# Performance work log

Measured on AMD Instinct MI355X. Metric: run time of the kernel, lower is better.

Reference implementation:

```python
import jax, jax.numpy as jnp
import numpy as np

K = 8              # kernel_size
C_IN = 3           # input_channels
HID = 256          # hidden_state_size
MID = 256          # mid_layer_size
N_MAIN = 4         # num_main_layers
N_CLS = 1000       # num_classes
N_PIX = K * K      # num_pixel_values
IN_VEC = 2 + 1 + N_PIX * C_IN + HID   # 451
OUT_VEC = 2 + 1 + HID                 # 259
B, H, W = 128, 256, 256


def _lin_init(k, fan_in, fan_out):
    kw, kb = jax.random.split(k)
    bound = 1.0 / np.sqrt(fan_in)
    w = jax.random.uniform(kw, (fan_in, fan_out), jnp.float32, -bound, bound)
    b = jax.random.uniform(kb, (fan_out,), jnp.float32, -bound, bound)
    return w, b


def setup_inputs() -> dict:
    key = jax.random.key(0)
    ks = jax.random.split(key, 16)
    image = jax.random.normal(ks[0], (B, C_IN, H, W), jnp.float32)
    locations = jax.random.uniform(ks[1], (B, 2), jnp.float32)
    scales = jax.random.uniform(ks[2], (B, 1), jnp.float32)
    hidden_state = jax.random.normal(ks[3], (B, HID), jnp.float32)
    w0, b0 = _lin_init(ks[4], IN_VEC, MID)
    rws, rbs = [], []
    for i in range(N_MAIN):
        w, b = _lin_init(jax.random.fold_in(ks[5], i), MID, MID)
        rws.append(w); rbs.append(b)
    rw = jnp.stack(rws); rb = jnp.stack(rbs)          # [4,MID,MID], [4,MID]
    wf, bf = _lin_init(ks[6], MID, OUT_VEC)
    cw0, cb0 = _lin_init(ks[7], HID, MID)
    crw, crb = _lin_init(ks[8], MID, MID)
    cw1, cb1 = _lin_init(ks[9], MID, N_CLS)
    return {"image": image, "locations": locations, "scales": scales,
            "hidden_state": hidden_state, "w0": w0, "b0": b0, "rw": rw,
            "rb": rb, "wf": wf, "bf": bf, "cw0": cw0, "cb0": cb0,
            "crw": crw, "crb": crb, "cw1": cw1, "cb1": cb1}


def fourier_interp_2d(image, sample_points):
    """Band-limited (NUDFT) interpolation of image at continuous points.
    image: [B,C,H,W]; sample_points: [B,N,2] in normalized [0,1) (ij order).
    Returns [B,N,C]."""
    Bsz, C, Hh, Ww = image.shape
    F = jnp.fft.fft2(image)                       # [B,C,H,W] complex
    fy = jnp.fft.fftfreq(Hh) * Hh                 # integer freqs [H]
    fx = jnp.fft.fftfreq(Ww) * Ww                 # integer freqs [W]
    y = sample_points[..., 0]                     # [B,N]
    x = sample_points[..., 1]
    two_pi_i = 2j * jnp.pi
    Ey = jnp.exp(two_pi_i * y[..., None] * fy)    # [B,N,H]
    Ex = jnp.exp(two_pi_i * x[..., None] * fx)    # [B,N,W]
    tmp = jnp.einsum('bchw,bnh->bcnw', F, Ey)     # dominant compute
    vals = jnp.einsum('bcnw,bnw->bcn', tmp, Ex).real / (Hh * Ww)
    return jnp.transpose(vals, (0, 2, 1))         # [B,N,C]


def reference(image, locations, scales, hidden_state,
              w0, b0, rw, rb, wf, bf, cw0, cb0, crw, crb, cw1, cb1):
    Bsz = image.shape[0]
    # base meshgrid: [K,K,2], ij indexing, values arange(K)/K
    g = jnp.arange(K, dtype=image.dtype) / K
    mesh = jnp.stack(jnp.meshgrid(g, g, indexing='ij'), axis=-1)  # [K,K,2]
    coords = mesh[None] - locations[:, None, None, :]             # [B,K,K,2]
    coords = coords * scales[:, None, None, :]
    coords = coords.reshape(Bsz, N_PIX, 2)
    pix = fourier_interp_2d(image, coords)                        # [B,N,C]
    pix = pix.reshape(Bsz, N_PIX * C_IN)
    inp = jnp.concatenate([locations, scales, pix, hidden_state], axis=-1)
    h = inp @ w0 + b0
    for i in range(N_MAIN):
        h = jax.nn.relu(h @ rw[i] + rb[i] + h)
    out = jnp.tanh(h @ wf + bf)                                   # [B,OUT_VEC]
    new_loc = locations + out[:, :2]
    new_scale = scales + out[:, 2:3]
    new_hidden = hidden_state + out[:, 3:]
    c = jax.nn.relu(new_hidden @ cw0 + cb0)
    c = jax.nn.relu(c @ crw + crb + c)
    preds = jax.nn.softmax(c @ cw1 + cb1, axis=-1)
    # concat all outputs: [B, 2+1+HID+N_CLS]
    return jnp.concatenate([new_loc, new_scale, new_hidden, preds], axis=-1)
```

## Files before the change

kernel.cpp:

```cpp
#include <hip/hip_runtime.h>
#include <math.h>

#define BB 128
#define OUTROW 1259

typedef float vf4 __attribute__((ext_vector_type(4)));

__device__ __forceinline__ ushort f2b(float x) {
    unsigned u = __float_as_uint(x);
    unsigned r = (u + 0x7FFFu + ((u >> 16) & 1u)) >> 16;
    return (ushort)r;
}
__device__ __forceinline__ uint pack2(float lo, float hi) {
    return (uint)f2b(lo) | ((uint)f2b(hi) << 16);
}
__device__ __forceinline__ float dot2bf(uint a, uint b, float c) {
    float d;
    asm("v_dot2_f32_bf16 %0, %1, %2, %3" : "=v"(d) : "v"(a), "v"(b), "v"(c));
    return d;
}

#define OFF_W0   0u
#define OFF_RW   122880u
#define OFF_CW0  385024u
#define OFF_CRW  450560u
#define OFF_WF   516096u
#define OFF_CW1  582656u
#define N_TOT    838656u

__device__ __forceinline__ void dirichlet_ab(float t, float& A, float& Bv) {
    float r = t - rintf(t);
    float s256 = sinpif(256.0f * r);
    Bv = s256 * (1.0f / 256.0f);
    if (fabsf(r) < 1e-6f) {
        A = 1.0f;
    } else {
        float sp = sinpif(r), cp = cospif(r);
        A = Bv * cp / sp;
    }
}

__global__ __launch_bounds__(256) void interp_convert_kernel(
    const float* __restrict__ image, const float* __restrict__ loc,
    const float* __restrict__ scl, float* __restrict__ pix,
    const float* __restrict__ w0, const float* __restrict__ rw,
    const float* __restrict__ wf, const float* __restrict__ cw0,
    const float* __restrict__ crw, const float* __restrict__ cw1,
    ushort* __restrict__ bfa)
{
    __shared__ float U[256 * 16];
    __shared__ float V[16 * 260];
    __shared__ float T[16 * 260];

    int bid = blockIdx.x;
    int tid = threadIdx.x;

    if (bid >= 384) {
        unsigned g = (unsigned)(bid - 384) * 256u + (unsigned)tid;
        for (unsigned i = g; i < N_TOT; i += 512u * 256u) {
            unsigned j = i;
            if (j < 122880u) {
                unsigned kp = j >> 9, r = j & 511u, c = r >> 1, k = 2u*kp + (r & 1u);
                bfa[OFF_W0 + j] = (k < 451u) ? f2b(w0[k * 256u + c]) : (ushort)0;
            } else if (j < 385024u) {
                unsigned jj = j - 122880u;
                unsigned kp = jj >> 9, r = jj & 511u, c = r >> 1, k = 2u*kp + (r & 1u);
                bfa[OFF_RW + jj] = f2b(rw[k * 256u + c]);
            } else if (j < 450560u) {
                unsigned jj = j - 385024u;
                unsigned kp = jj >> 9, r = jj & 511u, c = r >> 1, k = 2u*kp + (r & 1u);
                bfa[OFF_CW0 + jj] = f2b(cw0[k * 256u + c]);
            } else if (j < 516096u) {
                unsigned jj = j - 450560u;
                unsigned kp = jj >> 9, r = jj & 511u, c = r >> 1, k = 2u*kp + (r & 1u);
                bfa[OFF_CRW + jj] = f2b(crw[k * 256u + c]);
            } else if (j < 582656u) {
                unsigned jj = j - 516096u;
                unsigned kp = jj / 520u, r = jj - kp * 520u, c = r >> 1, k = 2u*kp + (r & 1u);
                bfa[OFF_WF + jj] = (c < 259u) ? f2b(wf[k * 259u + c]) : (ushort)0;
            } else {
                unsigned jj = j - 582656u;
                unsigned kp = jj / 2000u, r = jj - kp * 2000u, c = r >> 1, k = 2u*kp + (r & 1u);
                bfa[OFF_CW1 + jj] = f2b(cw1[k * 1000u + c]);
            }
        }
        return;
    }

    int b = bid / 3, c = bid % 3;
    float l0 = loc[2 * b], l1 = loc[2 * b + 1], sc = scl[b];

    {
        int p = tid;
        float tp = (float)p * (1.0f / 256.0f);
        #pragma unroll
        for (int iy = 0; iy < 8; ++iy) {
            float A, Bv;
            float y = ((float)iy * 0.125f - l0) * sc;
            dirichlet_ab(y - tp, A, Bv);
            int w = iy >> 1, o = iy & 1;
            U[p * 16 + w * 4 + o] = A;
            U[p * 16 + w * 4 + 2 + o] = Bv;
            float x = ((float)iy * 0.125f - l1) * sc;
            dirichlet_ab(x - tp, A, Bv);
            V[iy * 260 + p] = A;
            V[(8 + iy) * 260 + p] = Bv;
        }
    }
    __syncthreads();

    int wave = tid >> 6, lane = tid & 63;
    const float* img = image + (size_t)(b * 3 + c) * 65536 + lane * 4;

    float aA0[4] = {0, 0, 0, 0}, aA1[4] = {0, 0, 0, 0};
    float aB0[4] = {0, 0, 0, 0}, aB1[4] = {0, 0, 0, 0};
    #pragma unroll 4
    for (int p = 0; p < 256; ++p) {
        vf4 v = __builtin_nontemporal_load((const vf4*)(img + p * 256));
        const float4 u = *(const float4*)(&U[p * 16 + wave * 4]);
        aA0[0] += u.x * v[0]; aA0[1] += u.x * v[1]; aA0[2] += u.x * v[2]; aA0[3] += u.x * v[3];
        aA1[0] += u.y * v[0]; aA1[1] += u.y * v[1]; aA1[2] += u.y * v[2]; aA1[3] += u.y * v[3];
        aB0[0] += u.z * v[0]; aB0[1] += u.z * v[1]; aB0[2] += u.z * v[2]; aB0[3] += u.z * v[3];
        aB1[0] += u.w * v[0]; aB1[1] += u.w * v[1]; aB1[2] += u.w * v[2]; aB1[3] += u.w * v[3];
    }
    int iy0 = wave * 2;
    int q0 = lane * 4;
    #pragma unroll
    for (int j = 0; j < 4; ++j) {
        T[iy0 * 260 + q0 + j]       = aA0[j];
        T[(iy0 + 1) * 260 + q0 + j] = aA1[j];
        T[(8 + iy0) * 260 + q0 + j]     = aB0[j];
        T[(8 + iy0 + 1) * 260 + q0 + j] = aB1[j];
    }
    __syncthreads();

    int n = tid >> 2, sub = tid & 3;
    int iy = n >> 3, ix = n & 7;
    float s = 0.f;
    #pragma unroll 8
    for (int i = 0; i < 64; ++i) {
        int q = sub + 4 * i;
        s += T[iy * 260 + q] * V[ix * 260 + q] - T[(8 + iy) * 260 + q] * V[(8 + ix) * 260 + q];
    }
    s += __shfl_xor(s, 1);
    s += __shfl_xor(s, 2);
    if (sub == 0) pix[(b * 64 + n) * 3 + c] = s;
}

__global__ __launch_bounds__(1024, 1) void mlp_fused(
    const float* __restrict__ loc, const float* __restrict__ scl,
    const float* __restrict__ hidden, const float* __restrict__ pix,
    const ushort* __restrict__ bfa,
    const float* __restrict__ b0, const float* __restrict__ rb,
    const float* __restrict__ bf, const float* __restrict__ cb0,
    const float* __restrict__ crb, const float* __restrict__ cb1,
    float* __restrict__ out)
{
    __shared__ float s_in[480];
    __shared__ float s_h[256];
    __shared__ float s_c[256];
    __shared__ float s_o[260];
    __shared__ float s_part[16 * 260];
    __shared__ float s_lg[1024];
    __shared__ uint  s_in2[240];
    __shared__ uint  s_hb2[128];
    __shared__ uint  s_cb2[128];
    __shared__ float s_b0[256], s_rb[1024], s_bf[260], s_cb0[256], s_crb[256], s_cb1[1000];
    __shared__ float s_red[32];

    int b = blockIdx.x, tid = threadIdx.x;
    int jg = tid & 63, sub = tid >> 6;
    int j4 = jg * 4;
    float* orow = out + (size_t)b * OUTROW;

    if (tid < 2) s_in[tid] = loc[2 * b + tid];
    if (tid == 2) s_in[2] = scl[b];
    if (tid >= 256 && tid < 448) s_in[3 + (tid - 256)] = pix[b * 192 + (tid - 256)];
    if (tid >= 512 && tid < 768) s_in[195 + (tid - 512)] = hidden[b * 256 + (tid - 512)];
    if (tid >= 768 && tid < 797) s_in[451 + (tid - 768)] = 0.f;
    if (tid < 256) s_b0[tid] = b0[tid];
    s_rb[tid] = rb[tid];
    if (tid < 259) s_bf[tid] = bf[tid];
    if (tid >= 256 && tid < 512) s_cb0[tid - 256] = cb0[tid - 256];
    if (tid >= 512 && tid < 768) s_crb[tid - 512] = crb[tid - 512];
    if (tid < 1000) s_cb1[tid] = cb1[tid];
    __syncthreads();
    if (tid < 240) s_in2[tid] = pack2(s_in[2 * tid], s_in[2 * tid + 1]);
    __syncthreads();

    const ushort* w0b  = bfa + OFF_W0;
    const ushort* rwb  = bfa + OFF_RW;
    const ushort* cw0b = bfa + OFF_CW0;
    const ushort* crwb = bfa + OFF_CRW;
    const ushort* wfb  = bfa + OFF_WF;
    const ushort* cw1b = bfa + OFF_CW1;

    {
        uint4 wv[15]; uint hv[15];
        #pragma unroll
        for (int t = 0; t < 15; ++t)
            wv[t] = *(const uint4*)(w0b + (size_t)(sub + 16 * t) * 512 + jg * 8);
        #pragma unroll
        for (int t = 0; t < 15; ++t) hv[t] = s_in2[sub + 16 * t];
        vf4 a = {0.f, 0.f, 0.f, 0.f};
        #pragma unroll
        for (int t = 0; t < 15; ++t) {
            a[0] = dot2bf(wv[t].x, hv[t], a[0]);
            a[1] = dot2bf(wv[t].y, hv[t], a[1]);
            a[2] = dot2bf(wv[t].z, hv[t], a[2]);
            a[3] = dot2bf(wv[t].w, hv[t], a[3]);
        }
        *(vf4*)(&s_part[sub * 256 + j4]) = a;
    }
    __syncthreads();
    if (tid < 256) {
        float v = s_b0[tid];
        #pragma unroll
        for (int s = 0; s < 16; ++s) v += s_part[s * 256 + tid];
        s_h[tid] = v;
        float v2 = __shfl_xor(v, 1);
        if (!(tid & 1)) s_hb2[tid >> 1] = pack2(v, v2);
    }
    __syncthreads();

    #pragma unroll 1
    for (int L = 0; L < 4; ++L) {
        const ushort* W = rwb + (size_t)L * 65536;
        {
            uint4 wv[8]; uint hv[8];
            #pragma unroll
            for (int t = 0; t < 8; ++t)
                wv[t] = *(const uint4*)(W + (size_t)(sub + 16 * t) * 512 + jg * 8);
            #pragma unroll
            for (int t = 0; t < 8; ++t) hv[t] = s_hb2[sub + 16 * t];
            vf4 a = {0.f, 0.f, 0.f, 0.f};
            #pragma unroll
            for (int t = 0; t < 8; ++t) {
                a[0] = dot2bf(wv[t].x, hv[t], a[0]);
                a[1] = dot2bf(wv[t].y, hv[t], a[1]);
                a[2] = dot2bf(wv[t].z, hv[t], a[2]);
                a[3] = dot2bf(wv[t].w, hv[t], a[3]);
            }
            *(vf4*)(&s_part[sub * 256 + j4]) = a;
        }
        __syncthreads();
        if (tid < 256) {
            float v = s_rb[L * 256 + tid] + s_h[tid];
            #pragma unroll
            for (int s = 0; s < 16; ++s) v += s_part[s * 256 + tid];
            v = fmaxf(v, 0.f);
            s_h[tid] = v;
            float v2 = __shfl_xor(v, 1);
            if (!(tid & 1)) s_hb2[tid >> 1] = pack2(v, v2);
        }
        __syncthreads();
    }

    {
        uint4 wv[8]; uint hv[8];
        #pragma unroll
        for (int t = 0; t < 8; ++t)
            wv[t] = *(const uint4*)(wfb + (size_t)(sub + 16 * t) * 520 + jg * 8);
        #pragma unroll
        for (int t = 0; t < 8; ++t) hv[t] = s_hb2[sub + 16 * t];
        vf4 a = {0.f, 0.f, 0.f, 0.f};
        #pragma unroll
        for (int t = 0; t < 8; ++t) {
            a[0] = dot2bf(wv[t].x, hv[t], a[0]);
            a[1] = dot2bf(wv[t].y, hv[t], a[1]);
            a[2] = dot2bf(wv[t].z, hv[t], a[2]);
            a[3] = dot2bf(wv[t].w, hv[t], a[3]);
        }
        *(vf4*)(&s_part[sub * 260 + j4]) = a;
        if (jg < 4) {
            float e = 0.f;
            #pragma unroll
            for (int t = 0; t < 8; ++t) {
                uint w = *(const uint*)(wfb + (size_t)(sub + 16 * t) * 520 + 512 + jg * 2);
                e = dot2bf(w, hv[t], e);
            }
            s_part[sub * 260 + 256 + jg] = e;
        }
    }
    __syncthreads();
    if (tid < 259) {
        float v = s_bf[tid];
        #pragma unroll
        for (int s = 0; s < 16; ++s) v += s_part[s * 260 + tid];
        s_o[tid] = tanhf(v);
    }
    __syncthreads();

    if (tid < 256) {
        float nh = s_in[195 + tid] + s_o[3 + tid];
        orow[3 + tid] = nh;
        s_h[tid] = nh;
        float v2 = __shfl_xor(nh, 1);
        if (!(tid & 1)) s_hb2[tid >> 1] = pack2(nh, v2);
    }
    if (tid == 256) orow[0] = s_in[0] + s_o[0];
    if (tid == 257) orow[1] = s_in[1] + s_o[1];
    if (tid == 258) orow[2] = s_in[2] + s_o[2];
    __syncthreads();

    {
        uint4 wv[8]; uint hv[8];
        #pragma unroll
        for (int t = 0; t < 8; ++t)
            wv[t] = *(const uint4*)(cw0b + (size_t)(sub + 16 * t) * 512 + jg * 8);
        #pragma unroll
        for (int t = 0; t < 8; ++t) hv[t] = s_hb2[sub + 16 * t];
        vf4 a = {0.f, 0.f, 0.f, 0.f};
        #pragma unroll
        for (int t = 0; t < 8; ++t) {
            a[0] = dot2bf(wv[t].x, hv[t], a[0]);
            a[1] = dot2bf(wv[t].y, hv[t], a[1]);
            a[2] = dot2bf(wv[t].z, hv[t], a[2]);
            a[3] = dot2bf(wv[t].w, hv[t], a[3]);
        }
        *(vf4*)(&s_part[sub * 256 + j4]) = a;
    }
    __syncthreads();
    if (tid < 256) {
        float v = s_cb0[tid];
        #pragma unroll
        for (int s = 0; s < 16; ++s) v += s_part[s * 256 + tid];
        v = fmaxf(v, 0.f);
        s_c[tid] = v;
        float v2 = __shfl_xor(v, 1);
        if (!(tid & 1)) s_cb2[tid >> 1] = pack2(v, v2);
    }
    __syncthreads();

    {
        uint4 wv[8]; uint hv[8];
        #pragma unroll
        for (int t = 0; t < 8; ++t)
            wv[t] = *(const uint4*)(crwb + (size_t)(sub + 16 * t) * 512 + jg * 8);
        #pragma unroll
        for (int t = 0; t < 8; ++t) hv[t] = s_cb2[sub + 16 * t];
        vf4 a = {0.f, 0.f, 0.f, 0.f};
        #pragma unroll
        for (int t = 0; t < 8; ++t) {
            a[0] = dot2bf(wv[t].x, hv[t], a[0]);
            a[1] = dot2bf(wv[t].y, hv[t], a[1]);
            a[2] = dot2bf(wv[t].z, hv[t], a[2]);
            a[3] = dot2bf(wv[t].w, hv[t], a[3]);
        }
        *(vf4*)(&s_part[sub * 256 + j4]) = a;
    }
    __syncthreads();
    if (tid < 256) {
        float v = s_crb[tid] + s_c[tid];
        #pragma unroll
        for (int s = 0; s < 16; ++s) v += s_part[s * 256 + tid];
        v = fmaxf(v, 0.f);
        float v2 = __shfl_xor(v, 1);
        if (!(tid & 1)) s_cb2[tid >> 1] = pack2(v, v2);
    }
    __syncthreads();

    int jg8 = tid & 127, sub8 = tid >> 7;
    int c4 = jg8 * 4;
    {
        uint4 wv[16]; uint hv[16];
        #pragma unroll
        for (int t = 0; t < 16; ++t)
            wv[t] = *(const uint4*)(cw1b + (size_t)(sub8 + 8 * t) * 2000 + c4 * 2);
        #pragma unroll
        for (int t = 0; t < 16; ++t) hv[t] = s_cb2[sub8 + 8 * t];
        vf4 a = {0.f, 0.f, 0.f, 0.f};
        #pragma unroll
        for (int t = 0; t < 16; ++t) {
            a[0] = dot2bf(wv[t].x, hv[t], a[0]);
            a[1] = dot2bf(wv[t].y, hv[t], a[1]);
            a[2] = dot2bf(wv[t].z, hv[t], a[2]);
            a[3] = dot2bf(wv[t].w, hv[t], a[3]);
        }
        *(vf4*)(&s_part[sub8 * 512 + c4]) = a;
    }
    __syncthreads();
    if (tid < 512) {
        float v = s_cb1[tid];
        #pragma unroll
        for (int s = 0; s < 8; ++s) v += s_part[s * 512 + tid];
        s_lg[tid] = v;
    }
    __syncthreads();

    {
        vf4 a = {0.f, 0.f, 0.f, 0.f};
        if (jg8 < 122) {
            uint4 wv[16]; uint hv[16];
            #pragma unroll
            for (int t = 0; t < 16; ++t)
                wv[t] = *(const uint4*)(cw1b + (size_t)(sub8 + 8 * t) * 2000 + (512 + c4) * 2);
            #pragma unroll
            for (int t = 0; t < 16; ++t) hv[t] = s_cb2[sub8 + 8 * t];
            #pragma unroll
            for (int t = 0; t < 16; ++t) {
                a[0] = dot2bf(wv[t].x, hv[t], a[0]);
                a[1] = dot2bf(wv[t].y, hv[t], a[1]);
                a[2] = dot2bf(wv[t].z, hv[t], a[2]);
                a[3] = dot2bf(wv[t].w, hv[t], a[3]);
            }
        }
        *(vf4*)(&s_part[sub8 * 512 + c4]) = a;
    }
    __syncthreads();
    if (tid < 488) {
        float v = s_cb1[512 + tid];
        #pragma unroll
        for (int s = 0; s < 8; ++s) v += s_part[s * 512 + tid];
        s_lg[512 + tid] = v;
    }
    __syncthreads();

    float lgv = (tid < 1000) ? s_lg[tid] : -1e30f;
    int lane = tid & 63, wid = tid >> 6;
    float m = lgv;
    #pragma unroll
    for (int off = 1; off < 64; off <<= 1) m = fmaxf(m, __shfl_xor(m, off));
    if (lane == 0) s_red[wid] = m;
    __syncthreads();
    m = s_red[0];
    #pragma unroll
    for (int w = 1; w < 16; ++w) m = fmaxf(m, s_red[w]);

    float e = (tid < 1000) ? expf(lgv - m) : 0.f;
    float lsum = e;
    #pragma unroll
    for (int off = 1; off < 64; off <<= 1) lsum += __shfl_xor(lsum, off);
    if (lane == 0) s_red[16 + wid] = lsum;
    __syncthreads();
    float total = 0.f;
    #pragma unroll
    for (int w = 0; w < 16; ++w) total += s_red[16 + w];

    if (tid < 1000) orow[259 + tid] = e / total;
}

extern "C" void kernel_launch(void* const* d_in, const int* in_sizes, int n_in,
                              void* d_out, int out_size, void* d_ws, size_t ws_size,
                              hipStream_t stream) {
    const float* image  = (const float*)d_in[0];
    const float* loc    = (const float*)d_in[1];
    const float* scl    = (const float*)d_in[2];
    const float* hidden = (const float*)d_in[3];
    const float* w0  = (const float*)d_in[4];
    const float* b0  = (const float*)d_in[5];
    const float* rw  = (const float*)d_in[6];
    const float* rb  = (const float*)d_in[7];
    const float* wf  = (const float*)d_in[8];
    const float* bf  = (const float*)d_in[9];
    const float* cw0 = (const float*)d_in[10];
    const float* cb0 = (const float*)d_in[11];
    const float* crw = (const float*)d_in[12];
    const float* crb = (const float*)d_in[13];
    const float* cw1 = (const float*)d_in[14];
    const float* cb1 = (const float*)d_in[15];

    float* ws   = (float*)d_ws;
    float* pix  = ws;
    ushort* bfa = (ushort*)(ws + 24576);

    hipLaunchKernelGGL(interp_convert_kernel, dim3(384 + 512), dim3(256), 0, stream,
                       image, loc, scl, pix, w0, rw, wf, cw0, crw, cw1, bfa);
    hipLaunchKernelGGL(mlp_fused, dim3(BB), dim3(1024), 0, stream,
                       loc, scl, hidden, pix, bfa,
                       b0, rb, bf, cb0, crb, cb1, (float*)d_out);
}
```

Baseline: 74.31 us.

## Split classifier logits and softmax into separate wider-grid kernels

Moves the final 256x1000 classifier matmul out of the per-batch fused MLP kernel into a logits kernel launched on a 128x8 grid, followed by a separate softmax kernel. The cw1 bf16 layout is padded to 1024 columns so each block reads aligned column slices. The goal is to spread the largest weight read across many more workgroups instead of 128 blocks each looping over all 1000 columns. In exchange it adds two kernel launches and global round-trips for the activations and logits.

```diff
diff --git a/kernel.cpp b/kernel.cpp
--- a/kernel.cpp
+++ b/kernel.cpp
@@ -26,7 +26,12 @@
 #define OFF_CRW  450560u
 #define OFF_WF   516096u
 #define OFF_CW1  582656u
-#define N_TOT    838656u
+#define N_TOT    844800u
+
+#define WS_PIX   0u
+#define WS_BFA   24576u
+#define WS_C1P   450048u
+#define WS_LG    466432u
 
 __device__ __forceinline__ void dirichlet_ab(float t, float& A, float& Bv) {
     float r = t - rintf(t);
@@ -57,8 +62,7 @@
 
     if (bid >= 384) {
         unsigned g = (unsigned)(bid - 384) * 256u + (unsigned)tid;
-        for (unsigned i = g; i < N_TOT; i += 512u * 256u) {
-            unsigned j = i;
+        for (unsigned j = g; j < N_TOT; j += 512u * 256u) {
             if (j < 122880u) {
                 unsigned kp = j >> 9, r = j & 511u, c = r >> 1, k = 2u*kp + (r & 1u);
                 bfa[OFF_W0 + j] = (k < 451u) ? f2b(w0[k * 256u + c]) : (ushort)0;
@@ -80,8 +84,8 @@
                 bfa[OFF_WF + jj] = (c < 259u) ? f2b(wf[k * 259u + c]) : (ushort)0;
             } else {
                 unsigned jj = j - 582656u;
-                unsigned kp = jj / 2000u, r = jj - kp * 2000u, c = r >> 1, k = 2u*kp + (r & 1u);
-                bfa[OFF_CW1 + jj] = f2b(cw1[k * 1000u + c]);
+                unsigned kp = jj / 2048u, r = jj - kp * 2048u, c = r >> 1, k = 2u*kp + (r & 1u);
+                bfa[OFF_CW1 + jj] = (c < 1000u) ? f2b(cw1[k * 1000u + c]) : (ushort)0;
             }
         }
         return;
@@ -147,26 +151,24 @@
     if (sub == 0) pix[(b * 64 + n) * 3 + c] = s;
 }
 
-__global__ __launch_bounds__(1024, 1) void mlp_fused(
+__global__ __launch_bounds__(1024, 1) void mlp_main(
     const float* __restrict__ loc, const float* __restrict__ scl,
     const float* __restrict__ hidden, const float* __restrict__ pix,
     const ushort* __restrict__ bfa,
     const float* __restrict__ b0, const float* __restrict__ rb,
     const float* __restrict__ bf, const float* __restrict__ cb0,
-    const float* __restrict__ crb, const float* __restrict__ cb1,
-    float* __restrict__ out)
+    const float* __restrict__ crb,
+    uint* __restrict__ c1p, float* __restrict__ out)
 {
     __shared__ float s_in[480];
     __shared__ float s_h[256];
     __shared__ float s_c[256];
     __shared__ float s_o[260];
     __shared__ float s_part[16 * 260];
-    __shared__ float s_lg[1024];
     __shared__ uint  s_in2[240];
     __shared__ uint  s_hb2[128];
     __shared__ uint  s_cb2[128];
-    __shared__ float s_b0[256], s_rb[1024], s_bf[260], s_cb0[256], s_crb[256], s_cb1[1000];
-    __shared__ float s_red[32];
+    __shared__ float s_b0[256], s_rb[1024], s_bf[260], s_cb0[256], s_crb[256];
 
     int b = blockIdx.x, tid = threadIdx.x;
     int jg = tid & 63, sub = tid >> 6;
@@ -183,7 +185,6 @@
     if (tid < 259) s_bf[tid] = bf[tid];
     if (tid >= 256 && tid < 512) s_cb0[tid - 256] = cb0[tid - 256];
     if (tid >= 512 && tid < 768) s_crb[tid - 512] = crb[tid - 512];
-    if (tid < 1000) s_cb1[tid] = cb1[tid];
     __syncthreads();
     if (tid < 240) s_in2[tid] = pack2(s_in[2 * tid], s_in[2 * tid + 1]);
     __syncthreads();
@@ -193,7 +194,6 @@
     const ushort* cw0b = bfa + OFF_CW0;
     const ushort* crwb = bfa + OFF_CRW;
     const ushort* wfb  = bfa + OFF_WF;
-    const ushort* cw1b = bfa + OFF_CW1;
 
     {
         uint4 wv[15]; uint hv[15];
@@ -356,67 +356,63 @@
         for (int s = 0; s < 16; ++s) v += s_part[s * 256 + tid];
         v = fmaxf(v, 0.f);
         float v2 = __shfl_xor(v, 1);
-        if (!(tid & 1)) s_cb2[tid >> 1] = pack2(v, v2);
-    }
-    __syncthreads();
-
-    int jg8 = tid & 127, sub8 = tid >> 7;
-    int c4 = jg8 * 4;
-    {
-        uint4 wv[16]; uint hv[16];
-        #pragma unroll
-        for (int t = 0; t < 16; ++t)
-            wv[t] = *(const uint4*)(cw1b + (size_t)(sub8 + 8 * t) * 2000 + c4 * 2);
-        #pragma unroll
-        for (int t = 0; t < 16; ++t) hv[t] = s_cb2[sub8 + 8 * t];
-        vf4 a = {0.f, 0.f, 0.f, 0.f};
-        #pragma unroll
-        for (int t = 0; t < 16; ++t) {
-            a[0] = dot2bf(wv[t].x, hv[t], a[0]);
-            a[1] = dot2bf(wv[t].y, hv[t], a[1]);
-            a[2] = dot2bf(wv[t].z, hv[t], a[2]);
-            a[3] = dot2bf(wv[t].w, hv[t], a[3]);
-        }
-        *(vf4*)(&s_part[sub8 * 512 + c4]) = a;
-    }
-    __syncthreads();
-    if (tid < 512) {
-        float v = s_cb1[tid];
-        #pragma unroll
-        for (int s = 0; s < 8; ++s) v += s_part[s * 512 + tid];
-        s_lg[tid] = v;
-    }
-    __syncthreads();
-
-    {
-        vf4 a = {0.f, 0.f, 0.f, 0.f};
-        if (jg8 < 122) {
-            uint4 wv[16]; uint hv[16];
-            #pragma unroll
-            for (int t = 0; t < 16; ++t)
-                wv[t] = *(const uint4*)(cw1b + (size_t)(sub8 + 8 * t) * 2000 + (512 + c4) * 2);
-            #pragma unroll
-            for (int t = 0; t < 16; ++t) hv[t] = s_cb2[sub8 + 8 * t];
-            #pragma unroll
-            for (int t = 0; t < 16; ++t) {
-                a[0] = dot2bf(wv[t].x, hv[t], a[0]);
-                a[1] = dot2bf(wv[t].y, hv[t], a[1]);
-                a[2] = dot2bf(wv[t].z, hv[t], a[2]);
-                a[3] = dot2bf(wv[t].w, hv[t], a[3]);
-            }
-        }
-        *(vf4*)(&s_part[sub8 * 512 + c4]) = a;
-    }
-    __syncthreads();
-    if (tid < 488) {
-        float v = s_cb1[512 + tid];
-        #pragma unroll
-        for (int s = 0; s < 8; ++s) v += s_part[s * 512 + tid];
-        s_lg[512 + tid] = v;
-    }
-    __syncthreads();
-
-    float lgv = (tid < 1000) ? s_lg[tid] : -1e30f;
+        if (!(tid & 1)) c1p[b * 128 + (tid >> 1)] = pack2(v, v2);
+    }
+}
+
+__global__ __launch_bounds__(1024, 1) void logits_kernel(
+    const uint* __restrict__ c1p, const ushort* __restrict__ bfa,
+    const float* __restrict__ cb1, float* __restrict__ lg)
+{
+    __shared__ uint  s_c2[128];
+    __shared__ float s_part[32 * 128];
+
+    const uint* cw1b = (const uint*)(bfa + OFF_CW1);
+
+    int b = blockIdx.x, s = blockIdx.y, tid = threadIdx.x;
+    if (tid < 128) s_c2[tid] = c1p[b * 128 + tid];
+    __syncthreads();
+
+    int cg = tid & 31, sub = tid >> 5;
+    int col0 = s * 128 + cg * 4;
+
+    uint4 wv[4]; uint hv[4];
+    #pragma unroll
+    for (int t = 0; t < 4; ++t)
+        wv[t] = *(const uint4*)(cw1b + (size_t)(sub + 32 * t) * 1024 + col0);
+    #pragma unroll
+    for (int t = 0; t < 4; ++t) hv[t] = s_c2[sub + 32 * t];
+    vf4 a = {0.f, 0.f, 0.f, 0.f};
+    #pragma unroll
+    for (int t = 0; t < 4; ++t) {
+        a[0] = dot2bf(wv[t].x, hv[t], a[0]);
+        a[1] = dot2bf(wv[t].y, hv[t], a[1]);
+        a[2] = dot2bf(wv[t].z, hv[t], a[2]);
+        a[3] = dot2bf(wv[t].w, hv[t], a[3]);
+    }
+    *(vf4*)(&s_part[sub * 128 + cg * 4]) = a;
+    __syncthreads();
+
+    if (tid < 128) {
+        int col = s * 128 + tid;
+        if (col < 1000) {
+            float v = cb1[col];
+            #pragma unroll
+            for (int ss = 0; ss < 32; ++ss) v += s_part[ss * 128 + tid];
+            lg[(size_t)b * 1024 + col] = v;
+        }
+    }
+}
+
+__global__ __launch_bounds__(1024) void softmax_kernel(
+    const float* __restrict__ lg, float* __restrict__ out)
+{
+    __shared__ float s_red[32];
+    int b = blockIdx.x, tid = threadIdx.x;
+    float* orow = out + (size_t)b * OUTROW;
+
+    float lgv = (tid < 1000) ? lg[(size_t)b * 1024 + tid] : -1e30f;
+
     int lane = tid & 63, wid = tid >> 6;
     float m = lgv;
     #pragma unroll
@@ -461,12 +457,18 @@
     const float* cb1 = (const float*)d_in[15];
 
     float* ws   = (float*)d_ws;
-    float* pix  = ws;
-    ushort* bfa = (ushort*)(ws + 24576);
+    float* pix  = ws + WS_PIX;
+    ushort* bfa = (ushort*)(ws + WS_BFA);
+    uint*  c1p  = (uint*)(ws + WS_C1P);
+    float* lg   = ws + WS_LG;
 
     hipLaunchKernelGGL(interp_convert_kernel, dim3(384 + 512), dim3(256), 0, stream,
                        image, loc, scl, pix, w0, rw, wf, cw0, crw, cw1, bfa);
-    hipLaunchKernelGGL(mlp_fused, dim3(BB), dim3(1024), 0, stream,
+    hipLaunchKernelGGL(mlp_main, dim3(BB), dim3(1024), 0, stream,
                        loc, scl, hidden, pix, bfa,
-                       b0, rb, bf, cb0, crb, cb1, (float*)d_out);
-}
+                       b0, rb, bf, cb0, crb, c1p, (float*)d_out);
+    hipLaunchKernelGGL(logits_kernel, dim3(BB, 8), dim3(1024), 0, stream,
+                       c1p, bfa, cb1, lg);
+    hipLaunchKernelGGL(softmax_kernel, dim3(BB), dim3(1024), 0, stream,
+                       lg, (float*)d_out);
+}
```

Measured after the change: 75.89 us. 2.1% more time.
